# Performance work log

Measured on AMD Instinct MI355X. Metric: run time of the kernel, lower is better.

## Reference

```python
import jax, jax.numpy as jnp
import numpy as np

B, T, S_ENC, H, V = 8, 128, 400, 256, 50257


def setup_inputs() -> dict:
    key = jax.random.key(0)
    ks = jax.random.split(key, 16)
    inp = {
        "input_tokens": jax.random.randint(ks[0], (B, S_ENC), 0, V),
        "context": jax.random.normal(ks[1], (B, T, H), dtype=jnp.float32),
        "decoder_input": jax.random.normal(ks[2], (B, T, H), dtype=jnp.float32),
        "decoder_output": jax.random.normal(ks[3], (B, T, H), dtype=jnp.float32),
        "vocab_dist": jax.random.uniform(ks[4], (B, T, V), dtype=jnp.float32),
        "attn_dist": jax.random.uniform(ks[5], (B, T, S_ENC), dtype=jnp.float32),
        "encoder_outputs": jax.random.normal(ks[6], (B, S_ENC, H), dtype=jnp.float32),
        # Linear(H, 1) params for the three p_gen projections
        "Wc": jax.random.normal(ks[7], (H, 1), dtype=jnp.float32) / np.sqrt(H),
        "bc": jnp.zeros((1,), dtype=jnp.float32),
        "Wo": jax.random.normal(ks[8], (H, 1), dtype=jnp.float32) / np.sqrt(H),
        "bo": jnp.zeros((1,), dtype=jnp.float32),
        "Wi": jax.random.normal(ks[9], (H, 1), dtype=jnp.float32) / np.sqrt(H),
        "bi": jnp.zeros((1,), dtype=jnp.float32),
    }
    return inp


def reference(input_tokens, context, decoder_input, decoder_output, vocab_dist,
              attn_dist, encoder_outputs, Wc, bc, Wo, bo, Wi, bi):
    # p_gen: sigmoid of sum of three Linear(H,1) projections -> [B, T, 1]
    p_gen = jax.nn.sigmoid(
        context @ Wc + bc + decoder_output @ Wo + bo + decoder_input @ Wi + bi
    )
    # copy distribution: scatter_add attn_dist into a [B, T, V] zeros tensor
    # along the vocab axis at the source token ids (broadcast over T).
    b_idx = jnp.arange(vocab_dist.shape[0])[:, None, None]   # [B,1,1]
    t_idx = jnp.arange(vocab_dist.shape[1])[None, :, None]   # [1,T,1]
    copy_dist = jnp.zeros_like(vocab_dist).at[
        b_idx, t_idx, input_tokens[:, None, :]
    ].add(attn_dist)
    # gated mix (same math as torch source: vocab_dist * p_gen + (1-p_gen) * log_softmax(copy))
    final_dist = vocab_dist * p_gen + (1.0 - p_gen) * jax.nn.log_softmax(copy_dist, axis=2)
    return final_dist
```

## Files before the change

kernel.cpp:

```cpp
#include <hip/hip_runtime.h>
#include <math.h>

#define B 8
#define T 128
#define S_ENC 400
#define H 256
#define V 50257
#define HASH_SZ 1024

typedef float vfloat4 __attribute__((ext_vector_type(4)));


__global__ __launch_bounds__(256) void build_kernel(
    const int* __restrict__ tokens,
    int* __restrict__ u, int* __restrict__ rnk, int* __restrict__ cnt)
{
    __shared__ int hk[HASH_SZ];
    __shared__ int hr[HASH_SZ];
    __shared__ int c;
    const int b = blockIdx.x, tid = threadIdx.x;

    for (int i = tid; i < HASH_SZ; i += 256) hk[i] = -1;
    if (tid == 0) c = 0;
    __syncthreads();

    for (int s = tid; s < S_ENC; s += 256) {
        const int tk = tokens[b * S_ENC + s];
        unsigned h = ((unsigned)tk * 2654435761u >> 16) & (HASH_SZ - 1);
        for (;;) {
            int prev = atomicCAS(&hk[h], -1, tk);
            if (prev == -1 || prev == tk) break;
            h = (h + 1) & (HASH_SZ - 1);
        }
    }
    __syncthreads();

    for (int i = tid; i < HASH_SZ; i += 256) {
        if (hk[i] != -1) {
            const int r = atomicAdd(&c, 1);
            hr[i] = r;
            u[b * S_ENC + r] = hk[i];
        }
    }
    __syncthreads();

    for (int s = tid; s < S_ENC; s += 256) {
        const int tk = tokens[b * S_ENC + s];
        unsigned h = ((unsigned)tk * 2654435761u >> 16) & (HASH_SZ - 1);
        while (hk[h] != tk) h = (h + 1) & (HASH_SZ - 1);
        rnk[b * S_ENC + s] = hr[h];
    }
    if (tid == 0) cnt[b] = c;
}

__global__ __launch_bounds__(256) void prep_kernel(
    const float* __restrict__ context,
    const float* __restrict__ dec_in,
    const float* __restrict__ dec_out,
    const float* __restrict__ attn,
    const float* __restrict__ Wc, const float* __restrict__ bc,
    const float* __restrict__ Wo, const float* __restrict__ bo,
    const float* __restrict__ Wi, const float* __restrict__ bi,
    const int* __restrict__ rnk, const int* __restrict__ cnt,
    float4* __restrict__ params, float* __restrict__ vs)
{
    __shared__ float val[S_ENC];
    __shared__ float s_pg[4], s_m[4], s_se[4];
    __shared__ float s_mb, s_q;
    const int bt   = blockIdx.x;
    const int b    = bt >> 7;
    const int tid  = threadIdx.x;
    const int lane = tid & 63;
    const int wave = tid >> 6;

    for (int i = tid; i < S_ENC; i += 256) val[i] = 0.0f;

    {
        float v = context[bt * H + tid] * Wc[tid]
                + dec_out[bt * H + tid] * Wo[tid]
                + dec_in [bt * H + tid] * Wi[tid];
        #pragma unroll
        for (int off = 32; off; off >>= 1) v += __shfl_down(v, off, 64);
        if (lane == 0) s_pg[wave] = v;
    }
    __syncthreads();

    for (int s = tid; s < S_ENC; s += 256)
        atomicAdd(&val[rnk[b * S_ENC + s]], attn[bt * S_ENC + s]);
    __syncthreads();

    const int n = cnt[b];
    {
        float m = 0.0f;
        for (int i = tid; i < n; i += 256) m = fmaxf(m, val[i]);
        #pragma unroll
        for (int off = 32; off; off >>= 1) m = fmaxf(m, __shfl_down(m, off, 64));
        if (lane == 0) s_m[wave] = m;
    }
    __syncthreads();
    if (tid == 0) s_mb = fmaxf(fmaxf(s_m[0], s_m[1]), fmaxf(s_m[2], s_m[3]));
    __syncthreads();
    {
        const float m = s_mb;
        float se = 0.0f;
        for (int i = tid; i < n; i += 256) se += expf(val[i] - m);
        #pragma unroll
        for (int off = 32; off; off >>= 1) se += __shfl_down(se, off, 64);
        if (lane == 0) s_se[wave] = se;
    }
    __syncthreads();
    if (tid == 0) {
        const float m   = s_mb;
        float se  = s_se[0] + s_se[1] + s_se[2] + s_se[3]
                  + (float)(V - n) * expf(-m);
        float lse = m + logf(se);
        float x   = s_pg[0] + s_pg[1] + s_pg[2] + s_pg[3]
                  + bc[0] + bo[0] + bi[0];
        float p   = 1.0f / (1.0f + expf(-x));
        float q   = 1.0f - p;
        params[bt] = make_float4(p, q * lse, q, 0.0f);
        s_q = q;
    }
    __syncthreads();
    const float q = s_q;
    for (int i = tid; i < n; i += 256) vs[bt * S_ENC + i] = q * val[i];
}

#define STASH_MAX 800

__global__ __launch_bounds__(256) void mix_kernel(
    const vfloat4* __restrict__ vocab,
    const float4*  __restrict__ params,
    const int*     __restrict__ u,
    const int*     __restrict__ cnt,
    const float*   __restrict__ vs,
    vfloat4* __restrict__ out)
{
    __shared__ int   s_d[STASH_MAX];
    __shared__ float s_v[STASH_MAX];
    __shared__ int   s_k;
    const int tid = threadIdx.x;
    const int idx = blockIdx.x * 256 + tid;
    const int e0  = blockIdx.x << 10;
    const int bt0 = e0 / V;
    const int btL = (e0 + 1023) / V;

    if (tid == 0) s_k = 0;
    vfloat4 v = __builtin_nontemporal_load(&vocab[idx]);
    __syncthreads();

    for (int r = bt0; r <= btL; ++r) {
        const int base = r * V;
        const int bb   = r >> 7;
        const int n    = cnt[bb];
        const int*   ub = u  + bb * S_ENC;
        const float* vb = vs + r  * S_ENC;
        for (int i = tid; i < n; i += 256) {
            const int d = base + ub[i] - e0;
            if ((unsigned)d < 1024u) {
                const int slot = atomicAdd(&s_k, 1);
                s_d[slot] = d;
                s_v[slot] = vb[i];
            }
        }
    }
    __syncthreads();

    vfloat4 o;
    const int eb = idx << 2;
    if (bt0 == btL) {
        const float4 P = params[bt0];
        o = v * P.x - P.y;
    } else {
        #pragma unroll
        for (int j = 0; j < 4; ++j) {
            const int bt = (eb + j) / V;
            const float4 P = params[bt];
            o[j] = v[j] * P.x - P.y;
        }
    }

    const int k  = s_k;
    const int my = eb - e0;
    for (int j = 0; j < k; ++j) {
        const int   d = s_d[j] - my;
        const float a = s_v[j];
        o[0] += (d == 0) ? a : 0.0f;
        o[1] += (d == 1) ? a : 0.0f;
        o[2] += (d == 2) ? a : 0.0f;
        o[3] += (d == 3) ? a : 0.0f;
    }
    __builtin_nontemporal_store(o, &out[idx]);
}

extern "C" void kernel_launch(void* const* d_in, const int* in_sizes, int n_in,
                              void* d_out, int out_size, void* d_ws, size_t ws_size,
                              hipStream_t stream) {
    const int*   tokens  = (const int*)  d_in[0];
    const float* context = (const float*)d_in[1];
    const float* dec_in  = (const float*)d_in[2];
    const float* dec_out = (const float*)d_in[3];
    const float* vocab   = (const float*)d_in[4];
    const float* attn    = (const float*)d_in[5];
    const float* Wc = (const float*)d_in[7];
    const float* bc = (const float*)d_in[8];
    const float* Wo = (const float*)d_in[9];
    const float* bo = (const float*)d_in[10];
    const float* Wi = (const float*)d_in[11];
    const float* bi = (const float*)d_in[12];

    float* out = (float*)d_out;
    char*  ws  = (char*)d_ws;
    float4* params = (float4*)ws;
    int*    u      = (int*)  (ws + 16384);
    int*    rnk    = (int*)  (ws + 29184);
    int*    cnt    = (int*)  (ws + 41984);
    float*  vs     = (float*)(ws + 42048);

    build_kernel<<<B, 256, 0, stream>>>(tokens, u, rnk, cnt);

    prep_kernel<<<B * T, 256, 0, stream>>>(context, dec_in, dec_out, attn,
                                           Wc, bc, Wo, bo, Wi, bi,
                                           rnk, cnt, params, vs);

    const int total4 = (B * T * V) / 4;
    mix_kernel<<<total4 / 256, 256, 0, stream>>>(
        (const vfloat4*)vocab, (const float4*)params, u, cnt, vs, (vfloat4*)out);
}
```

Before: 389.9 us.

## Scatter copy values into dense shared tile instead of per-thread stash scan

The mix kernel used to append matching copy entries to a shared stash with atomics, and then every thread scanned the whole stash with compares. It now writes the copy values straight into a dense shared tile indexed by element offset and adds them with one vector read per quad. Each block also handles 2048 elements (two float4 per thread) with bounds guards, which halves the number of per-row token scans across blocks. The change removes the O(k) compare loop per thread in exchange for zeroing a shared tile and some extra predication.

```diff
diff --git a/kernel.cpp b/kernel.cpp
--- a/kernel.cpp
+++ b/kernel.cpp
@@ -7,6 +7,10 @@
 #define H 256
 #define V 50257
 #define HASH_SZ 1024
+#define NTOT (B * T * V)
+#define TOTAL4 (NTOT / 4)
+#define EPB 2048
+#define QPB (EPB / 4)
 
 typedef float vfloat4 __attribute__((ext_vector_type(4)));
 
@@ -126,8 +130,6 @@
     for (int i = tid; i < n; i += 256) vs[bt * S_ENC + i] = q * val[i];
 }
 
-#define STASH_MAX 800
-
 __global__ __launch_bounds__(256) void mix_kernel(
     const vfloat4* __restrict__ vocab,
     const float4*  __restrict__ params,
@@ -136,61 +138,74 @@
     const float*   __restrict__ vs,
     vfloat4* __restrict__ out)
 {
-    __shared__ int   s_d[STASH_MAX];
-    __shared__ float s_v[STASH_MAX];
-    __shared__ int   s_k;
+    __shared__ float tile[EPB];
     const int tid = threadIdx.x;
-    const int idx = blockIdx.x * 256 + tid;
-    const int e0  = blockIdx.x << 10;
+    const int q0  = blockIdx.x * QPB + tid;
+    const int q1  = q0 + 256;
+    const int e0  = blockIdx.x * EPB;
+    const int eL  = min(e0 + EPB - 1, NTOT - 1);
     const int bt0 = e0 / V;
-    const int btL = (e0 + 1023) / V;
-
-    if (tid == 0) s_k = 0;
-    vfloat4 v = __builtin_nontemporal_load(&vocab[idx]);
+    const int btL = eL / V;
+
+    const bool p0 = q0 < TOTAL4;
+    const bool p1 = q1 < TOTAL4;
+    vfloat4 v0 = {0.f, 0.f, 0.f, 0.f}, v1 = {0.f, 0.f, 0.f, 0.f};
+    if (p0) v0 = __builtin_nontemporal_load(&vocab[q0]);
+    if (p1) v1 = __builtin_nontemporal_load(&vocab[q1]);
+
+    vfloat4* tv = (vfloat4*)tile;
+    const vfloat4 z = {0.f, 0.f, 0.f, 0.f};
+    tv[tid]       = z;
+    tv[tid + 256] = z;
     __syncthreads();
 
     for (int r = bt0; r <= btL; ++r) {
-        const int base = r * V;
+        const int base = r * V - e0;
         const int bb   = r >> 7;
         const int n    = cnt[bb];
         const int*   ub = u  + bb * S_ENC;
         const float* vb = vs + r  * S_ENC;
         for (int i = tid; i < n; i += 256) {
-            const int d = base + ub[i] - e0;
-            if ((unsigned)d < 1024u) {
-                const int slot = atomicAdd(&s_k, 1);
-                s_d[slot] = d;
-                s_v[slot] = vb[i];
+            const int d = base + ub[i];
+            if ((unsigned)d < (unsigned)EPB) tile[d] = vb[i];
+        }
+    }
+    __syncthreads();
+
+    if (p0) {
+        const int e = q0 << 2;
+        vfloat4 o;
+        const int a = e / V, b2 = (e + 3) / V;
+        if (a == b2) {
+            const float4 P = params[a];
+            o = v0 * P.x - P.y;
+        } else {
+            #pragma unroll
+            for (int j = 0; j < 4; ++j) {
+                const float4 P = params[(e + j) / V];
+                o[j] = v0[j] * P.x - P.y;
             }
         }
-    }
-    __syncthreads();
-
-    vfloat4 o;
-    const int eb = idx << 2;
-    if (bt0 == btL) {
-        const float4 P = params[bt0];
-        o = v * P.x - P.y;
-    } else {
-        #pragma unroll
-        for (int j = 0; j < 4; ++j) {
-            const int bt = (eb + j) / V;
-            const float4 P = params[bt];
-            o[j] = v[j] * P.x - P.y;
-        }
-    }
-
-    const int k  = s_k;
-    const int my = eb - e0;
-    for (int j = 0; j < k; ++j) {
-        const int   d = s_d[j] - my;
-        const float a = s_v[j];
-        o[0] += (d == 0) ? a : 0.0f;
-        o[1] += (d == 1) ? a : 0.0f;
-        o[2] += (d == 2) ? a : 0.0f;
-        o[3] += (d == 3) ? a : 0.0f;
-    }
-    __builtin_nontemporal_store(o, &out[idx]);
+        o += tv[tid];
+        __builtin_nontemporal_store(o, &out[q0]);
+    }
+    if (p1) {
+        const int e = q1 << 2;
+        vfloat4 o;
+        const int a = e / V, b2 = (e + 3) / V;
+        if (a == b2) {
+            const float4 P = params[a];
+            o = v1 * P.x - P.y;
+        } else {
+            #pragma unroll
+            for (int j = 0; j < 4; ++j) {
+                const float4 P = params[(e + j) / V];
+                o[j] = v1[j] * P.x - P.y;
+            }
+        }
+        o += tv[tid + 256];
+        __builtin_nontemporal_store(o, &out[q1]);
+    }
 }
 
 extern "C" void kernel_launch(void* const* d_in, const int* in_sizes, int n_in,
@@ -223,7 +238,7 @@
                                            Wc, bc, Wo, bo, Wi, bi,
                                            rnk, cnt, params, vs);
 
-    const int total4 = (B * T * V) / 4;
-    mix_kernel<<<total4 / 256, 256, 0, stream>>>(
+    const int nb = (TOTAL4 + QPB - 1) / QPB;
+    mix_kernel<<<nb, 256, 0, stream>>>(
         (const vfloat4*)vocab, (const float4*)params, u, cnt, vs, (vfloat4*)out);
 }
```

After: 369.6 us. 1.05x faster.
